# Kernel optimization log

Hardware: AMD Instinct MI355X
Metric: run time of the kernel (lower is better)

## Reference

```python
import jax, jax.numpy as jnp
import numpy as np

DIM = 1024
IMG_H, IMG_W = 512, 1408
CROP = 224
IMAGE_ORDER = (2, 0, 1, 5, 3, 4)
B, NC, NB = 2, 6, 32


def setup_inputs():
    key = jax.random.key(0)
    ks = jax.random.split(key, 12)
    camera_imgs = jax.random.normal(ks[0], (B, NC, 3, IMG_H, IMG_W), jnp.float32)
    u = jax.random.uniform(ks[1], (B, NB, 9), dtype=jnp.float32)
    centers = jnp.stack([u[..., 0] * 45.0 + 5.0,
                         (u[..., 1] - 0.5) * 40.0,
                         (u[..., 2] - 0.5) * 4.0], -1)
    pred_boxes = jnp.concatenate([centers, u[..., 3:] * 2.0], -1)  # [B,NB,9]
    K = np.array([[500., 0., IMG_W / 2.], [0., 500., IMG_H / 2.], [0., 0., 1.]])
    R_l2c = np.array([[0., -1., 0.], [0., 0., -1.], [1., 0., 0.]])  # lidar->camera axes
    mats = np.zeros((NC, 4, 4), np.float32)
    for c in range(NC):
        yaw = 2.0 * np.pi * c / NC
        Rz = np.array([[np.cos(yaw), -np.sin(yaw), 0.], [np.sin(yaw), np.cos(yaw), 0.], [0., 0., 1.]])
        mats[c, :3, :3] = K @ R_l2c @ Rz.T
        mats[c, 3, 3] = 1.0
    lidar2image = jnp.broadcast_to(jnp.asarray(mats), (B, NC, 4, 4))
    eye4 = jnp.eye(4, dtype=jnp.float32)
    img_aug_matrix = jnp.broadcast_to(eye4, (B, NC, 4, 4))
    lidar_aug_matrix = jnp.broadcast_to(eye4, (B, 4, 4))
    momentum = jnp.float32(0.5)
    box_default_dim = jax.random.normal(ks[2], (1, DIM), jnp.float32)
    theta_w = jnp.zeros((4, 9), jnp.float32)  # zero-init as in torch code
    theta_b = jnp.array([1., 0., 0., 1.], jnp.float32)

    def cw(k, shape):
        fan = shape[1] * shape[2] * shape[3]
        return jax.random.normal(k, shape, jnp.float32) * (2.0 / fan) ** 0.5
    conv1 = cw(ks[3], (64, 3, 7, 7))
    conv2 = cw(ks[4], (256, 64, 3, 3))
    conv3 = cw(ks[5], (DIM, 256, 3, 3))
    pos_embed = jax.random.normal(ks[6], (50, DIM), jnp.float32) * 0.02
    s = DIM ** -0.5
    wq = jax.random.normal(ks[7], (DIM, DIM), jnp.float32) * s
    wk = jax.random.normal(ks[8], (DIM, DIM), jnp.float32) * s
    wv = jax.random.normal(ks[9], (DIM, DIM), jnp.float32) * s
    wo = jax.random.normal(ks[10], (DIM, DIM), jnp.float32) * s
    return dict(camera_imgs=camera_imgs, pred_boxes=pred_boxes,
                img_aug_matrix=img_aug_matrix, lidar_aug_matrix=lidar_aug_matrix,
                lidar2image=lidar2image, momentum=momentum,
                box_default_dim=box_default_dim, theta_w=theta_w, theta_b=theta_b,
                conv1=conv1, conv2=conv2, conv3=conv3, pos_embed=pos_embed,
                wq=wq, wk=wk, wv=wv, wo=wo)


def _project(pred_boxes, lidar_aug_matrix, lidar2image, img_aug_matrix):
    # returns vu [B,NC,NB,2] = (row, col) pixel coords, on_img [B,NC,NB]
    def per_b(boxes, la, l2i, aug):
        c = boxes[:, :3] - la[:3, 3]                       # [NB,3]
        c = jnp.linalg.inv(la[:3, :3]) @ c.T               # [3,NB]
        c = l2i[:, :3, :3] @ c + l2i[:, :3, 3:4]           # [NC,3,NB]
        z = jnp.clip(c[:, 2], 1e-5, 1e5)
        xy = c[:, :2] / z[:, None]
        c = jnp.concatenate([xy, z[:, None]], 1)
        c = aug[:, :3, :3] @ c + aug[:, :3, 3:4]
        uv = c[:, :2].transpose(0, 2, 1)                   # [NC,NB,2] (col,row)
        vu = uv[..., ::-1]                                 # (row,col)
        on = (vu[..., 0] < IMG_H) & (vu[..., 0] >= 0) & (vu[..., 1] < IMG_W) & (vu[..., 1] >= 0)
        return vu, on
    return jax.vmap(per_b)(pred_boxes, lidar_aug_matrix, lidar2image, img_aug_matrix)


def _base_grid(h, w):
    # torch affine_grid align_corners=False pixel-center coords
    xs = (2.0 * jnp.arange(w) + 1.0) / w - 1.0
    ys = (2.0 * jnp.arange(h) + 1.0) / h - 1.0
    gx, gy = jnp.meshgrid(xs, ys)  # [h,w]
    return jnp.stack([gx, gy, jnp.ones_like(gx)], -1)  # [h,w,3]


def _grid_sample(img, grid):
    # img [C,H,W]; grid [...,2] xy in [-1,1]; bilinear, zeros padding, align_corners=False
    C, H, W = img.shape
    ix = ((grid[..., 0] + 1.0) * W - 1.0) / 2.0
    iy = ((grid[..., 1] + 1.0) * H - 1.0) / 2.0
    x0 = jnp.floor(ix); y0 = jnp.floor(iy)
    x1 = x0 + 1.0; y1 = y0 + 1.0
    wx = ix - x0; wy = iy - y0

    def gather(xx, yy):
        xi = jnp.clip(xx, 0, W - 1).astype(jnp.int32)
        yi = jnp.clip(yy, 0, H - 1).astype(jnp.int32)
        valid = (xx >= 0) & (xx <= W - 1) & (yy >= 0) & (yy <= H - 1)
        return img[:, yi, xi] * valid.astype(img.dtype)  # [C, ...]
    v00 = gather(x0, y0); v01 = gather(x1, y0)
    v10 = gather(x0, y1); v11 = gather(x1, y1)
    return (v00 * (1 - wx) * (1 - wy) + v01 * wx * (1 - wy)
            + v10 * (1 - wx) * wy + v11 * wx * wy)  # [C, ...]


def _clip_head(x, conv1, conv2, conv3, pos_embed, wq, wk, wv, wo):
    dn = ('NCHW', 'OIHW', 'NCHW')
    h = jax.nn.relu(jax.lax.conv_general_dilated(x, conv1, (4, 4), 'SAME', dimension_numbers=dn))
    h = jax.nn.relu(jax.lax.conv_general_dilated(h, conv2, (4, 4), 'SAME', dimension_numbers=dn))
    h = jax.nn.relu(jax.lax.conv_general_dilated(h, conv3, (2, 2), 'SAME', dimension_numbers=dn))  # [M,D,7,7]
    tok = h.reshape(h.shape[0], DIM, 49).transpose(0, 2, 1)              # [M,49,D]
    tok = jnp.concatenate([tok.mean(1, keepdims=True), tok], 1) + pos_embed  # [M,50,D]
    q = tok[:, :1] @ wq
    k = tok @ wk
    v = tok @ wv
    attn = jax.nn.softmax((q @ k.transpose(0, 2, 1)) * (DIM ** -0.5), -1)
    return ((attn @ v) @ wo)[:, 0]  # [M,D]


def reference(camera_imgs, pred_boxes, img_aug_matrix, lidar_aug_matrix, lidar2image,
              momentum, box_default_dim, theta_w, theta_b,
              conv1, conv2, conv3, pos_embed, wq, wk, wv, wo):
    N = B * NB
    vu, on_img = _project(pred_boxes, lidar_aug_matrix, lidar2image, img_aug_matrix)  # [B,NC,NB,2],[B,NC,NB]
    boxes_flat = pred_boxes.reshape(N, 9)
    rot = jnp.tanh(boxes_flat @ theta_w.T + theta_b).reshape(N, 2, 2)   # theta_rot MLP
    ty = vu[..., 0] / IMG_H * 2.0 - 1.0                                 # [B,NC,NB]
    tx = vu[..., 1] / IMG_W * 2.0 - 1.0
    pos = jnp.stack([tx, ty], -1).transpose(0, 2, 1, 3).reshape(N, NC, 2)
    theta = jnp.concatenate([jnp.broadcast_to(rot[:, None], (N, NC, 2, 2)),
                             pos[..., None]], -1)                        # [N,NC,2,3]
    base = _base_grid(CROP, CROP)                                        # [224,224,3]
    grids = jnp.einsum('hwk,ncjk->nchwj', base, theta)                   # [N,NC,224,224,2]
    grids = grids.reshape(B, NB, NC, CROP, CROP, 2)
    crops = []
    for b in range(B):
        for c in range(NC):
            smp = _grid_sample(camera_imgs[b, c], grids[b, :, c])        # [3,NB,224,224]
            crops.append(smp.transpose(1, 0, 2, 3))
    crops = jnp.stack(crops).reshape(B, NC, NB, 3, CROP, CROP)
    crops = crops.transpose(0, 2, 1, 3, 4, 5).reshape(N * NC, 3, CROP, CROP)
    emb = _clip_head(crops, conv1, conv2, conv3, pos_embed, wq, wk, wv, wo).reshape(N, NC, DIM)
    valid = on_img.transpose(0, 2, 1).reshape(N, NC)
    e = jnp.broadcast_to(box_default_dim, (N, DIM))
    for c in IMAGE_ORDER:  # sequential EMA over cameras, skipping off-image ones
        m = valid[:, c:c + 1]
        e = jnp.where(m, momentum * e + (1.0 - momentum) * emb[:, c], e)
    return e  # [N, DIM]
```

## Files before the change

### kernel.cpp

```cpp
#include <hip/hip_runtime.h>
#include <hip/hip_bf16.h>

#define DIMN 1024
#define IMG_H 512
#define IMG_W 1408
#define CROPN 224
#define NCAM 6
#define NBOXB 32
#define NBOX 64
#define NIMG 384

typedef __hip_bfloat16 bf16;
typedef unsigned short u16;
typedef float f32x4 __attribute__((ext_vector_type(4)));
typedef short bf16x8 __attribute__((ext_vector_type(8)));
typedef u16 u16x4 __attribute__((ext_vector_type(4)));
typedef u16 u16x8 __attribute__((ext_vector_type(8)));

__device__ __forceinline__ float b2f(bf16 x) { return __bfloat162float(x); }
__device__ __forceinline__ u16 f2us(float x) {
  bf16 h = __float2bfloat16(x);
  return *(u16*)&h;
}
__device__ __forceinline__ bf16x8 as_b(u16x8 x) {
  union { u16x8 u; bf16x8 b; } c; c.u = x; return c.b;
}

__global__ void k_w1r(const float* __restrict__ in, u16* __restrict__ out) {
  int idx = blockIdx.x * 256 + threadIdx.x;
  if (idx >= 64 * 224) return;
  int oc = idx / 224, t = idx % 224;
  int r = t >> 5, u = t & 31, kw = u >> 2, ch = u & 3;
  u16 v = (kw < 7 && ch < 3) ? f2us(in[((oc * 3 + ch) * 7 + r) * 7 + kw]) : (u16)0;
  out[(((oc >> 4) * 28 + (t >> 3)) * 16 + (oc & 15)) * 8 + (t & 7)] = v;
}
__global__ void k_w2r(const float* __restrict__ in, u16* __restrict__ out) {
  int idx = blockIdx.x * 256 + threadIdx.x;
  if (idx >= 256 * 576) return;
  int oc = idx / 576, t = idx % 576;
  int rk = t >> 6, ic = t & 63, r = rk / 3, kw = rk % 3;
  out[idx] = f2us(in[((oc * 64 + ic) * 3 + r) * 3 + kw]);
}
__global__ void k_w3r(const float* __restrict__ in, u16* __restrict__ out) {
  int idx = blockIdx.x * 256 + threadIdx.x;
  if (idx >= 1024 * 2304) return;
  int oc = idx / 2304, t = idx % 2304;
  int rk = t >> 8, ic = t & 255, r = rk / 3, kw = rk % 3;
  u16 v = f2us(in[((oc * 256 + ic) * 3 + r) * 3 + kw]);
  int ocb = oc >> 4, mm = oc & 15, kb = t >> 3, kj = t & 7;
  out[(((size_t)ocb * 288 + kb) * 16 + mm) * 8 + kj] = v;
}
__global__ void k_transpose_t(const float* __restrict__ w, float* __restrict__ wt) {
  __shared__ float tile[32][33];
  int x = blockIdx.x * 32 + threadIdx.x;
  for (int j = threadIdx.y; j < 32; j += 8)
    tile[j][threadIdx.x] = w[(size_t)(blockIdx.y * 32 + j) * 1024 + x];
  __syncthreads();
  int x2 = blockIdx.y * 32 + threadIdx.x;
  for (int j = threadIdx.y; j < 32; j += 8)
    wt[(size_t)(blockIdx.x * 32 + j) * 1024 + x2] = tile[threadIdx.x][j];
}

__global__ void k_proj(const float* __restrict__ boxes, const float* __restrict__ la_m,
                       const float* __restrict__ l2i, const float* __restrict__ aug,
                       const float* __restrict__ tw, const float* __restrict__ tb,
                       float* __restrict__ theta_out, int* __restrict__ valid_out) {
  int t = threadIdx.x;
  if (t >= NIMG) return;
  int n = t / NCAM, cam = t % NCAM;
  int b = n / NBOXB, nb = n % NBOXB;

  float la[4][4];
  for (int r = 0; r < 4; r++)
    for (int c = 0; c < 4; c++) la[r][c] = la_m[b * 16 + r * 4 + c];
  float a00=la[0][0],a01=la[0][1],a02=la[0][2];
  float a10=la[1][0],a11=la[1][1],a12=la[1][2];
  float a20=la[2][0],a21=la[2][1],a22=la[2][2];
  float c00 =  a11*a22 - a12*a21;
  float c01 = -(a10*a22 - a12*a20);
  float c02 =  a10*a21 - a11*a20;
  float det = a00*c00 + a01*c01 + a02*c02;
  float id = 1.0f / det;
  float inv[3][3];
  inv[0][0] = c00*id;                 inv[0][1] = -(a01*a22-a02*a21)*id;  inv[0][2] =  (a01*a12-a02*a11)*id;
  inv[1][0] = c01*id;                 inv[1][1] =  (a00*a22-a02*a20)*id;  inv[1][2] = -(a00*a12-a02*a10)*id;
  inv[2][0] = c02*id;                 inv[2][1] = -(a00*a21-a01*a20)*id;  inv[2][2] =  (a00*a11-a01*a10)*id;

  float bx[9];
  for (int i = 0; i < 9; i++) bx[i] = boxes[(b * NBOXB + nb) * 9 + i];
  float c0[3] = { bx[0]-la[0][3], bx[1]-la[1][3], bx[2]-la[2][3] };
  float c1[3];
  for (int r = 0; r < 3; r++) c1[r] = inv[r][0]*c0[0] + inv[r][1]*c0[1] + inv[r][2]*c0[2];

  const float* M = l2i + (size_t)(b * NCAM + cam) * 16;
  float p[3];
  for (int r = 0; r < 3; r++)
    p[r] = M[r*4+0]*c1[0] + M[r*4+1]*c1[1] + M[r*4+2]*c1[2] + M[r*4+3];
  float z = fminf(fmaxf(p[2], 1e-5f), 100000.0f);
  float x = p[0] / z, y = p[1] / z;
  const float* A = aug + (size_t)(b * NCAM + cam) * 16;
  float u = A[0]*x + A[1]*y + A[2]*z + A[3];
  float v = A[4]*x + A[5]*y + A[6]*z + A[7];

  int on = (v < (float)IMG_H) && (v >= 0.0f) && (u < (float)IMG_W) && (u >= 0.0f);
  float ty = v / (float)IMG_H * 2.0f - 1.0f;
  float tx = u / (float)IMG_W * 2.0f - 1.0f;

  float s[4];
  for (int j = 0; j < 4; j++) {
    float acc = tb[j];
    for (int i = 0; i < 9; i++) acc += tw[j * 9 + i] * bx[i];
    s[j] = tanhf(acc);
  }
  float* o = theta_out + t * 6;
  o[0] = s[0]; o[1] = s[1]; o[2] = tx;
  o[3] = s[2]; o[4] = s[3]; o[5] = ty;
  valid_out[t] = on;
}

#define HALO_PX 1356
__global__ void k_zero_halo(u16x4* __restrict__ c) {
  int t = blockIdx.x * 256 + threadIdx.x;
  int i = t / HALO_PX;
  if (i >= NIMG) return;
  int r = t % HALO_PX;
  int ph, pw;
  if (r < 684) {
    int rr = r / 228;
    ph = (rr == 0) ? 0 : (rr == 1 ? 225 : 226);
    pw = r % 228;
  } else {
    int q = r - 684;
    ph = 1 + q / 3;
    int s = q % 3;
    pw = (s == 0) ? 0 : (s == 1 ? 225 : 226);
  }
  c[(size_t)i * 228 * 228 + ph * 228 + pw] = (u16x4){0, 0, 0, 0};
}

__global__ __launch_bounds__(256) void k_sample(const float* __restrict__ imgs,
                                                const float* __restrict__ theta,
                                                u16* __restrict__ crops) {
  int idx = blockIdx.x * 256 + threadIdx.x;
  int i = idx / (CROPN * CROPN);
  int rem = idx - i * (CROPN * CROPN);
  int yy = rem / CROPN, xx = rem % CROPN;
  const float* th = theta + i * 6;
  float gx = (2.0f * xx + 1.0f) / (float)CROPN - 1.0f;
  float gy = (2.0f * yy + 1.0f) / (float)CROPN - 1.0f;
  float grid_x = th[0]*gx + th[1]*gy + th[2];
  float grid_y = th[3]*gx + th[4]*gy + th[5];
  float ix = ((grid_x + 1.0f) * (float)IMG_W - 1.0f) * 0.5f;
  float iy = ((grid_y + 1.0f) * (float)IMG_H - 1.0f) * 0.5f;
  float x0 = floorf(ix), y0 = floorf(iy);
  float wx = ix - x0, wy = iy - y0;
  int cam = i % NCAM, b = i / (NBOXB * NCAM);
  const float* base = imgs + (size_t)(b * NCAM + cam) * 3 * IMG_H * IMG_W;

  float xf[2] = { x0, x0 + 1.0f };
  float yf[2] = { y0, y0 + 1.0f };
  float wxa[2] = { 1.0f - wx, wx };
  float wya[2] = { 1.0f - wy, wy };
  int   xi[2], yi[2], vx[2], vy[2];
  for (int j = 0; j < 2; j++) {
    vx[j] = (xf[j] >= 0.0f) && (xf[j] <= (float)(IMG_W - 1));
    vy[j] = (yf[j] >= 0.0f) && (yf[j] <= (float)(IMG_H - 1));
    xi[j] = (int)fminf(fmaxf(xf[j], 0.0f), (float)(IMG_W - 1));
    yi[j] = (int)fminf(fmaxf(yf[j], 0.0f), (float)(IMG_H - 1));
  }
  float res[3];
  #pragma unroll
  for (int ch = 0; ch < 3; ch++) {
    const float* cp = base + (size_t)ch * IMG_H * IMG_W;
    float r = 0.0f;
    #pragma unroll
    for (int jy = 0; jy < 2; jy++)
      #pragma unroll
      for (int jx = 0; jx < 2; jx++) {
        float val = (vx[jx] && vy[jy]) ? cp[yi[jy] * IMG_W + xi[jx]] : 0.0f;
        r += val * wxa[jx] * wya[jy];
      }
    res[ch] = r;
  }
  u16x4 st = { f2us(res[0]), f2us(res[1]), f2us(res[2]), 0 };
  *(u16x4*)(crops + ((size_t)i * 228 * 228 + (size_t)(yy + 1) * 228 + (xx + 1)) * 4) = st;
}


#define C1_GROUPS 34
__global__ __launch_bounds__(256) void k_conv1m(const u16* __restrict__ X,
                                                const u16* __restrict__ W,
                                                u16* __restrict__ out) {
  __shared__ u16x8 sX[C1_GROUPS * 64];
  int blk = blockIdx.x;
  int i = blk / 14, rg = blk % 14;
  int tid = threadIdx.x, wv = tid >> 6, lane = tid & 63;
  int m = lane & 15, quad = lane >> 4;

  const u16* src = X + ((size_t)i * 51984 + (size_t)(rg * 16) * 228) * 4;
  #pragma unroll
  for (int j = 0; j < 9; j++) {
    int g = wv + j * 4;
    if (g < C1_GROUPS) {
      int c = g * 64 + lane;
      int cc = c < 2166 ? c : 2165;
      __builtin_amdgcn_global_load_lds(
          (const __attribute__((address_space(1))) void*)(src + (size_t)cc * 8),
          (__attribute__((address_space(3))) void*)(sX + g * 64),
          16, 0, 0);
    }
  }
  __syncthreads();

  int col[4];
  #pragma unroll
  for (int nt = 0; nt < 4; nt++) col[nt] = nt * 16 + m;
  f32x4 acc[4][4];
  #pragma unroll
  for (int t = 0; t < 4; t++)
    #pragma unroll
    for (int nt = 0; nt < 4; nt++) acc[t][nt] = (f32x4){0.f, 0.f, 0.f, 0.f};

  #pragma unroll
  for (int r = 0; r < 7; r++) {
    bf16x8 a[4];
    #pragma unroll
    for (int t = 0; t < 4; t++)
      a[t] = as_b(*(const u16x8*)(W + (size_t)(((t * 28 + r * 4 + quad) * 16 + m) * 8)));
    int lrow = wv * 4 + r;
    #pragma unroll
    for (int nt = 0; nt < 4; nt++) {
      int cl = col[nt] < 56 ? col[nt] : 55;
      bf16x8 bfr = as_b(sX[lrow * 114 + cl * 2 + quad]);
      #pragma unroll
      for (int t = 0; t < 4; t++)
        acc[t][nt] = __builtin_amdgcn_mfma_f32_16x16x32_bf16(a[t], bfr, acc[t][nt], 0, 0, 0);
    }
  }
  int oh = rg * 4 + wv;
  #pragma unroll
  for (int nt = 0; nt < 4; nt++) {
    if (col[nt] < 56) {
      int n = oh * 56 + col[nt];
      #pragma unroll
      for (int t = 0; t < 4; t++) {
        u16x4 st;
        #pragma unroll
        for (int r4 = 0; r4 < 4; r4++) st[r4] = f2us(fmaxf(acc[t][nt][r4], 0.f));
        *(u16x4*)(out + ((size_t)i * 3136 + n) * 64 + t * 16 + quad * 4) = st;
      }
    }
  }
}

__global__ __launch_bounds__(256) void k_conv2m(const u16* __restrict__ X,
                                                const u16* __restrict__ W,
                                                u16* __restrict__ out) {
  int blk = blockIdx.x;
  int i = blk >> 2, og = blk & 3;
  int oc0 = og * 64;
  int tid = threadIdx.x, wv = tid >> 6, lane = tid & 63;
  int m = lane & 15, quad = lane >> 4;
  int narr[4];
  const u16* bp[4];
  #pragma unroll
  for (int nt = 0; nt < 4; nt++) {
    int n = wv * 64 + nt * 16 + m;
    narr[nt] = n;
    int nc = n < 196 ? n : 195;
    int oh = nc / 14, ow = nc - oh * 14;
    bp[nt] = X + ((size_t)i * 3136 + (size_t)(oh * 4) * 56 + ow * 4) * 64 + quad * 8;
  }
  f32x4 acc[4][4];
  #pragma unroll
  for (int t = 0; t < 4; t++)
    #pragma unroll
    for (int nt = 0; nt < 4; nt++) acc[t][nt] = (f32x4){0.f, 0.f, 0.f, 0.f};

  #pragma unroll
  for (int s = 0; s < 18; s++) {
    const int rk = s >> 1, r = rk / 3, kw = rk % 3;
    const int boff = ((r * 56 + kw) * 64 + (s & 1) * 32);
    bf16x8 a[4];
    #pragma unroll
    for (int t = 0; t < 4; t++)
      a[t] = as_b(*(const u16x8*)(W + (size_t)(oc0 + t * 16 + m) * 576 + s * 32 + quad * 8));
    #pragma unroll
    for (int nt = 0; nt < 4; nt++) {
      bf16x8 bfr = as_b(*(const u16x8*)(bp[nt] + boff));
      #pragma unroll
      for (int t = 0; t < 4; t++)
        acc[t][nt] = __builtin_amdgcn_mfma_f32_16x16x32_bf16(a[t], bfr, acc[t][nt], 0, 0, 0);
    }
  }
  #pragma unroll
  for (int nt = 0; nt < 4; nt++) {
    int n = narr[nt];
    if (n < 196) {
      #pragma unroll
      for (int t = 0; t < 4; t++) {
        u16x4 st;
        #pragma unroll
        for (int r4 = 0; r4 < 4; r4++) st[r4] = f2us(fmaxf(acc[t][nt][r4], 0.f));
        *(u16x4*)(out + ((size_t)i * 196 + n) * 256 + oc0 + t * 16 + quad * 4) = st;
      }
    }
  }
}

__global__ __launch_bounds__(512, 2) void k_conv3m(const u16* __restrict__ X,
                                                   const u16* __restrict__ W,
                                                   float* __restrict__ out3) {
  __shared__ u16x8 sX8[6688];
  int bid = blockIdx.x;
  int og = (bid >> 2) & 1;
  int i  = (bid >> 3) * 4 + (bid & 3);
  int tid = threadIdx.x;

  const u16* src = X + (size_t)i * (196 * 256);
  u16x8 tmp[13];
  #pragma unroll
  for (int j = 0; j < 13; j++) {
    int c = tid + j * 512;
    int cc = c < 6272 ? c : 6271;
    tmp[j] = *(const u16x8*)(src + (size_t)cc * 8);
  }
  #pragma unroll
  for (int j = 0; j < 13; j++) {
    int c = tid + j * 512;
    int p = c >> 5, kc = c & 31;
    int ih = p / 14, iw = p - ih * 14;
    int gsw = ((iw >> 1) - (ih >> 1)) & 7;
    sX8[(c & ~31) | (kc ^ gsw)] = tmp[j];
  }
  if (tid < 32) sX8[6656 + tid] = (u16x8){0,0,0,0,0,0,0,0};
  __syncthreads();

  int wv = tid >> 6, lane = tid & 63;
  int m = lane & 15, quad = lane >> 4;
  int ocw = og * 512 + wv * 64;
  int narr[4], oh2[4], ow2[4];
  #pragma unroll
  for (int nt = 0; nt < 4; nt++) {
    int n = nt * 16 + m;
    narr[nt] = n;
    int nc = n < 49 ? n : 48;
    int oh = nc / 7, ow = nc - oh * 7;
    oh2[nt] = oh * 2; ow2[nt] = ow * 2;
  }
  f32x4 acc[4][4];
  #pragma unroll
  for (int t = 0; t < 4; t++)
    #pragma unroll
    for (int nt = 0; nt < 4; nt++) acc[t][nt] = (f32x4){0.f, 0.f, 0.f, 0.f};

  const u16* wbase = W + (size_t)(ocw >> 4) * (288 * 128) + m * 8;

  int bc[4], bk[4];
  auto set_bparams = [&](int rk) {
    const int r = rk / 3, kw = rk % 3;
    #pragma unroll
    for (int nt = 0; nt < 4; nt++) {
      int ih = oh2[nt] + r, iw = ow2[nt] + kw;
      bool valid = (narr[nt] < 49) && (ih < 14) && (iw < 14);
      int p = ih * 14 + iw;
      bc[nt] = valid ? p * 32 : 6656;
      bk[nt] = valid ? (((iw >> 1) - (ih >> 1)) & 7) : 0;
    }
  };
  auto loadA = [&](int t, int s) {
    return as_b(*(const u16x8*)(wbase + (size_t)(t * 288 + 4 * s + quad) * 128));
  };
  auto loadB = [&](int nt, int q4) {
    return as_b(sX8[bc[nt] + ((q4 + quad) ^ bk[nt])]);
  };

  bf16x8 A_[3][4], B_[2][4];
  set_bparams(0);
  #pragma unroll
  for (int t = 0; t < 4; t++) {
    A_[0][t] = loadA(t, 0);
    A_[1][t] = loadA(t, 1);
  }
  #pragma unroll
  for (int nt = 0; nt < 4; nt++) B_[0][nt] = loadB(nt, 0);

  #pragma unroll
  for (int s = 0; s < 72; s++) {
    if (s + 2 < 72) {
      #pragma unroll
      for (int t = 0; t < 4; t++) A_[(s + 2) % 3][t] = loadA(t, s + 2);
    }
    if (s + 1 < 72) {
      if (((s + 1) & 7) == 0) set_bparams((s + 1) >> 3);
      #pragma unroll
      for (int nt = 0; nt < 4; nt++) B_[(s + 1) & 1][nt] = loadB(nt, ((s + 1) & 7) * 4);
    }
    #pragma unroll
    for (int nt = 0; nt < 4; nt++)
      #pragma unroll
      for (int t = 0; t < 4; t++)
        acc[t][nt] = __builtin_amdgcn_mfma_f32_16x16x32_bf16(A_[s % 3][t], B_[s & 1][nt], acc[t][nt], 0, 0, 0);
  }

  #pragma unroll
  for (int nt = 0; nt < 4; nt++) {
    int n = narr[nt];
    if (n < 49) {
      #pragma unroll
      for (int t = 0; t < 4; t++) {
        f32x4 o;
        #pragma unroll
        for (int r4 = 0; r4 < 4; r4++) o[r4] = fmaxf(acc[t][nt][r4], 0.f);
        *(f32x4*)(out3 + ((size_t)i * 49 + n) * DIMN + ocw + t * 16 + quad * 4) = o;
      }
    }
  }
}

__global__ __launch_bounds__(256) void k_tok(const float* __restrict__ h,
                                             const float* __restrict__ pos,
                                             float* __restrict__ tok) {
  int blk = blockIdx.x;
  int i = blk / 50, t = blk % 50;
  int d = threadIdx.x * 4;
  float4 val;
  if (t == 0) {
    float sx = 0, sy = 0, sz = 0, sw = 0;
    for (int p = 0; p < 49; p++) {
      float4 v = *(const float4*)(h + ((size_t)i * 49 + p) * DIMN + d);
      sx += v.x; sy += v.y; sz += v.z; sw += v.w;
    }
    const float inv49 = 1.0f / 49.0f;
    val.x = sx * inv49; val.y = sy * inv49; val.z = sz * inv49; val.w = sw * inv49;
  } else {
    val = *(const float4*)(h + ((size_t)i * 49 + (t - 1)) * DIMN + d);
  }
  float4 pe = *(const float4*)(pos + (size_t)t * DIMN + d);
  float4 o; o.x = val.x + pe.x; o.y = val.y + pe.y; o.z = val.z + pe.z; o.w = val.w + pe.w;
  *(float4*)(tok + ((size_t)i * 50 + t) * DIMN + d) = o;
}

__global__ __launch_bounds__(256) void k_matvec2(const float* __restrict__ vecs, int vstride,
                                                 const float* __restrict__ M,
                                                 float* __restrict__ out) {
  __shared__ float s_v[4][DIMN];
  int i0 = blockIdx.x * 4;
  int h = blockIdx.y;
  for (int e = threadIdx.x; e < 4 * DIMN; e += 256)
    s_v[e >> 10][e & 1023] = vecs[(size_t)(i0 + (e >> 10)) * vstride + (e & 1023)];
  __syncthreads();
  int d0 = h * 512 + threadIdx.x * 2;
  float2 acc[4] = {{0,0},{0,0},{0,0},{0,0}};
  for (int e = 0; e < DIMN; e++) {
    float2 w = *(const float2*)(M + (size_t)e * DIMN + d0);
    #pragma unroll
    for (int im = 0; im < 4; im++) {
      float x = s_v[im][e];
      acc[im].x += x * w.x; acc[im].y += x * w.y;
    }
  }
  #pragma unroll
  for (int im = 0; im < 4; im++)
    *(float2*)(out + (size_t)(i0 + im) * DIMN + d0) = acc[im];
}

__global__ __launch_bounds__(256) void k_attn(const float* __restrict__ tok,
                                              const float* __restrict__ a1,
                                              float* __restrict__ tvec) {
  __shared__ float s_a[DIMN];
  __shared__ float s_sc[50];
  __shared__ float s_at[50];
  int i = blockIdx.x;
  for (int e = threadIdx.x; e < DIMN; e += 256) s_a[e] = a1[(size_t)i * DIMN + e];
  __syncthreads();
  int wave = threadIdx.x >> 6, lane = threadIdx.x & 63;
  for (int t = wave; t < 50; t += 4) {
    const float* tr = tok + ((size_t)i * 50 + t) * DIMN;
    float p = 0.0f;
    for (int mm = 0; mm < 16; mm++) {
      int e = lane + mm * 64;
      p += tr[e] * s_a[e];
    }
    for (int off = 32; off > 0; off >>= 1) p += __shfl_down(p, off, 64);
    if (lane == 0) s_sc[t] = p * 0.03125f;
  }
  __syncthreads();
  if (threadIdx.x == 0) {
    float mx = s_sc[0];
    for (int t = 1; t < 50; t++) mx = fmaxf(mx, s_sc[t]);
    float sum = 0.0f;
    for (int t = 0; t < 50; t++) { float ex = expf(s_sc[t] - mx); s_at[t] = ex; sum += ex; }
    float inv = 1.0f / sum;
    for (int t = 0; t < 50; t++) s_at[t] *= inv;
  }
  __syncthreads();
  int d0 = threadIdx.x * 4;
  float ax = 0, ay = 0, az = 0, aw = 0;
  for (int t = 0; t < 50; t++) {
    float at = s_at[t];
    float4 tv = *(const float4*)(tok + ((size_t)i * 50 + t) * DIMN + d0);
    ax += at * tv.x; ay += at * tv.y; az += at * tv.z; aw += at * tv.w;
  }
  float4 o; o.x = ax; o.y = ay; o.z = az; o.w = aw;
  *(float4*)(tvec + (size_t)i * DIMN + d0) = o;
}

__global__ void k_final(const float* __restrict__ emb,
                        const int* __restrict__ valid,
                        const float* __restrict__ bdd,
                        const float* __restrict__ momp,
                        float* __restrict__ out) {
  int n = blockIdx.x;
  int d0 = threadIdx.x * 4;
  float mom = momp[0];
  float e[4];
  #pragma unroll
  for (int j = 0; j < 4; j++) e[j] = bdd[d0 + j];
  const int order[6] = {2, 0, 1, 5, 3, 4};
  #pragma unroll
  for (int s = 0; s < 6; s++) {
    int c = order[s];
    int i = n * NCAM + c;
    if (valid[i]) {
      const float* er = emb + (size_t)i * DIMN + d0;
      #pragma unroll
      for (int j = 0; j < 4; j++) e[j] = mom * e[j] + (1.0f - mom) * er[j];
    }
  }
  #pragma unroll
  for (int j = 0; j < 4; j++) out[(size_t)n * DIMN + d0 + j] = e[j];
}

extern "C" void kernel_launch(void* const* d_in, const int* in_sizes, int n_in,
                              void* d_out, int out_size, void* d_ws, size_t ws_size,
                              hipStream_t stream) {
  const float* in_cam = (const float*)d_in[0];
  const float* in_box = (const float*)d_in[1];
  const float* in_aug = (const float*)d_in[2];
  const float* in_la  = (const float*)d_in[3];
  const float* in_l2i = (const float*)d_in[4];
  const float* in_mom = (const float*)d_in[5];
  const float* in_bdd = (const float*)d_in[6];
  const float* in_tw  = (const float*)d_in[7];
  const float* in_tb  = (const float*)d_in[8];
  const float* in_c1  = (const float*)d_in[9];
  const float* in_c2  = (const float*)d_in[10];
  const float* in_c3  = (const float*)d_in[11];
  const float* in_pe  = (const float*)d_in[12];
  const float* in_wq  = (const float*)d_in[13];
  const float* in_wk  = (const float*)d_in[14];
  const float* in_wv  = (const float*)d_in[15];
  const float* in_wo  = (const float*)d_in[16];

  char* base = (char*)d_ws;
  size_t off = 0;
  auto carve = [&](size_t bytes) -> char* {
    char* p = base + off;
    off += (bytes + 255) & ~(size_t)255;
    return p;
  };
  float* theta   = (float*)carve((size_t)NIMG * 6 * 4);
  int*   valid   = (int*)carve((size_t)NIMG * 4);
  float* qbuf    = (float*)carve((size_t)NIMG * DIMN * 4);
  float* a1buf   = (float*)carve((size_t)NIMG * DIMN * 4);
  float* tvbuf   = (float*)carve((size_t)NIMG * DIMN * 4);
  float* ctxbuf  = (float*)carve((size_t)NIMG * DIMN * 4);
  float* embbuf  = (float*)carve((size_t)NIMG * DIMN * 4);
  float* wkT_f   = (float*)carve((size_t)DIMN * DIMN * 4);
  u16*   W1r     = (u16*)carve((size_t)64 * 224 * 2);
  u16*   W2r     = (u16*)carve((size_t)256 * 576 * 2);
  u16*   W3r     = (u16*)carve((size_t)1024 * 2304 * 2);
  u16*   c2o     = (u16*)carve((size_t)NIMG * 196 * 256 * 2);
  char*  R1      = carve((size_t)NIMG * 228 * 228 * 4 * 2);
  u16*   c1o     = (u16*)carve((size_t)NIMG * 3136 * 64 * 2);
  u16*   crops   = (u16*)R1;
  float* conv3o  = (float*)R1;
  float* tok     = (float*)(R1 + (size_t)NIMG * 49 * DIMN * 4);

  k_w1r<<<56, 256, 0, stream>>>(in_c1, W1r);
  k_w2r<<<576, 256, 0, stream>>>(in_c2, W2r);
  k_w3r<<<9216, 256, 0, stream>>>(in_c3, W3r);
  k_transpose_t<<<dim3(32, 32), dim3(32, 8), 0, stream>>>(in_wk, wkT_f);

  k_proj<<<1, 384, 0, stream>>>(in_box, in_la, in_l2i, in_aug, in_tw, in_tb, theta, valid);
  k_zero_halo<<<(NIMG * HALO_PX + 255) / 256, 256, 0, stream>>>((u16x4*)crops);
  k_sample<<<(NIMG * CROPN * CROPN) / 256, 256, 0, stream>>>(in_cam, theta, crops);
  k_conv1m<<<NIMG * 14, 256, 0, stream>>>(crops, W1r, c1o);
  k_conv2m<<<NIMG * 4, 256, 0, stream>>>(c1o, W2r, c2o);
  k_conv3m<<<768, 512, 0, stream>>>(c2o, W3r, conv3o);
  k_tok<<<NIMG * 50, 256, 0, stream>>>(conv3o, in_pe, tok);
  k_matvec2<<<dim3(96, 2), 256, 0, stream>>>(tok, 50 * DIMN, in_wq, qbuf);
  k_matvec2<<<dim3(96, 2), 256, 0, stream>>>(qbuf, DIMN, wkT_f, a1buf);
  k_attn<<<NIMG, 256, 0, stream>>>(tok, a1buf, tvbuf);
  k_matvec2<<<dim3(96, 2), 256, 0, stream>>>(tvbuf, DIMN, in_wv, ctxbuf);
  k_matvec2<<<dim3(96, 2), 256, 0, stream>>>(ctxbuf, DIMN, in_wo, embbuf);
  k_final<<<NBOX, 256, 0, stream>>>(embbuf, valid, in_bdd, in_mom, (float*)d_out);
}
```

Measured before the change: 986.0 us.

## Stage conv2 input in swizzled LDS with MFMA-friendly weight layout

conv2 is restructured so each block covers one image and a band of output rows for all 256 channels. It loads the relevant input rows into LDS with an XOR swizzle and reads weights from a new blocked layout in place of the old strided global gathers. Triple-buffered A/B register prefetch is added. conv3 gets a 16-way swizzle and precomputed per-tap offsets so B-parameter math no longer runs in the main loop. The cost is more registers for the offset tables, which may reduce occupancy.

```diff
diff --git a/kernel.cpp b/kernel.cpp
--- a/kernel.cpp
+++ b/kernel.cpp
@@ -39,7 +39,8 @@
   if (idx >= 256 * 576) return;
   int oc = idx / 576, t = idx % 576;
   int rk = t >> 6, ic = t & 63, r = rk / 3, kw = rk % 3;
-  out[idx] = f2us(in[((oc * 64 + ic) * 3 + r) * 3 + kw]);
+  u16 v = f2us(in[((oc * 64 + ic) * 3 + r) * 3 + kw]);
+  out[(((oc >> 4) * 72 + (t >> 3)) * 16 + (oc & 15)) * 8 + (t & 7)] = v;
 }
 __global__ void k_w3r(const float* __restrict__ in, u16* __restrict__ out) {
   int idx = blockIdx.x * 256 + threadIdx.x;
@@ -253,56 +254,98 @@
   }
 }
 
-__global__ __launch_bounds__(256) void k_conv2m(const u16* __restrict__ X,
-                                                const u16* __restrict__ W,
-                                                u16* __restrict__ out) {
-  int blk = blockIdx.x;
-  int i = blk >> 2, og = blk & 3;
-  int oc0 = og * 64;
+__global__ __launch_bounds__(256, 3) void k_conv2m(const u16* __restrict__ X,
+                                                   const u16* __restrict__ W,
+                                                   u16* __restrict__ out) {
+  __shared__ u16x8 s2[3136];
+  int bid = blockIdx.x;
+  int i = bid / 7, ohg = bid % 7;
   int tid = threadIdx.x, wv = tid >> 6, lane = tid & 63;
   int m = lane & 15, quad = lane >> 4;
-  int narr[4];
-  const u16* bp[4];
-  #pragma unroll
-  for (int nt = 0; nt < 4; nt++) {
-    int n = wv * 64 + nt * 16 + m;
-    narr[nt] = n;
-    int nc = n < 196 ? n : 195;
-    int oh = nc / 14, ow = nc - oh * 14;
-    bp[nt] = X + ((size_t)i * 3136 + (size_t)(oh * 4) * 56 + ow * 4) * 64 + quad * 8;
-  }
-  f32x4 acc[4][4];
+
+  const u16* src = X + ((size_t)i * 3136 + 8 * ohg * 56) * 64;
+  u16x8 tmp[13];
+  #pragma unroll
+  for (int j = 0; j < 13; j++) {
+    int c = tid + j * 256;
+    int cc = c < 3136 ? c : 3135;
+    tmp[j] = *(const u16x8*)(src + (size_t)cc * 8);
+  }
+  #pragma unroll
+  for (int j = 0; j < 13; j++) {
+    int c = tid + j * 256;
+    int cc = c < 3136 ? c : 3135;
+    int pixel = cc >> 3;
+    int li = pixel / 56, iw = pixel - li * 56;
+    int g = (14 * (li >> 2) + (iw >> 2)) & 15;
+    s2[(cc & ~15) | ((cc ^ g) & 15)] = tmp[j];
+  }
+  __syncthreads();
+
+  int nl[2], pk2[9][2];
+  #pragma unroll
+  for (int nt = 0; nt < 2; nt++) {
+    int n = nt * 16 + m;
+    nl[nt] = n;
+    int nc = n < 28 ? n : 27;
+    int ohl = nc / 14, ow = nc - ohl * 14;
+    int g = nc & 15;
+    #pragma unroll
+    for (int rk = 0; rk < 9; rk++) {
+      int r = rk / 3, kw = rk % 3;
+      int pixel = (ohl * 4 + r) * 56 + (ow * 4 + kw);
+      int cb = pixel * 8;
+      int base2 = (cb & ~15) | ((cb & 8) ^ (g & 8));
+      pk2[rk][nt] = base2 | (g & 7);
+    }
+  }
+  f32x4 acc[4][2];
   #pragma unroll
   for (int t = 0; t < 4; t++)
     #pragma unroll
-    for (int nt = 0; nt < 4; nt++) acc[t][nt] = (f32x4){0.f, 0.f, 0.f, 0.f};
+    for (int nt = 0; nt < 2; nt++) acc[t][nt] = (f32x4){0.f, 0.f, 0.f, 0.f};
+
+  const u16* wbase = W + (size_t)(wv * 4) * (72 * 128) + m * 8;
+  auto loadA = [&](int t, int s) {
+    return as_b(*(const u16x8*)(wbase + (size_t)(t * 72 + s * 4 + quad) * 128));
+  };
+  auto loadB = [&](int nt, int s) {
+    int pkv = pk2[s >> 1][nt];
+    int sub = (s & 1) * 4 + quad;
+    return as_b(s2[(pkv & ~7) | (sub ^ (pkv & 7))]);
+  };
+
+  bf16x8 A_[3][4], B_[3][2];
+  #pragma unroll
+  for (int t = 0; t < 4; t++) { A_[0][t] = loadA(t, 0); A_[1][t] = loadA(t, 1); }
+  #pragma unroll
+  for (int nt = 0; nt < 2; nt++) { B_[0][nt] = loadB(nt, 0); B_[1][nt] = loadB(nt, 1); }
 
   #pragma unroll
   for (int s = 0; s < 18; s++) {
-    const int rk = s >> 1, r = rk / 3, kw = rk % 3;
-    const int boff = ((r * 56 + kw) * 64 + (s & 1) * 32);
-    bf16x8 a[4];
-    #pragma unroll
-    for (int t = 0; t < 4; t++)
-      a[t] = as_b(*(const u16x8*)(W + (size_t)(oc0 + t * 16 + m) * 576 + s * 32 + quad * 8));
-    #pragma unroll
-    for (int nt = 0; nt < 4; nt++) {
-      bf16x8 bfr = as_b(*(const u16x8*)(bp[nt] + boff));
+    if (s + 2 < 18) {
+      #pragma unroll
+      for (int t = 0; t < 4; t++) A_[(s + 2) % 3][t] = loadA(t, s + 2);
+      #pragma unroll
+      for (int nt = 0; nt < 2; nt++) B_[(s + 2) % 3][nt] = loadB(nt, s + 2);
+    }
+    #pragma unroll
+    for (int nt = 0; nt < 2; nt++)
       #pragma unroll
       for (int t = 0; t < 4; t++)
-        acc[t][nt] = __builtin_amdgcn_mfma_f32_16x16x32_bf16(a[t], bfr, acc[t][nt], 0, 0, 0);
-    }
-  }
-  #pragma unroll
-  for (int nt = 0; nt < 4; nt++) {
-    int n = narr[nt];
-    if (n < 196) {
+        acc[t][nt] = __builtin_amdgcn_mfma_f32_16x16x32_bf16(A_[s % 3][t], B_[s % 3][nt], acc[t][nt], 0, 0, 0);
+  }
+
+  #pragma unroll
+  for (int nt = 0; nt < 2; nt++) {
+    if (nl[nt] < 28) {
+      int n = ohg * 28 + nl[nt];
       #pragma unroll
       for (int t = 0; t < 4; t++) {
         u16x4 st;
         #pragma unroll
         for (int r4 = 0; r4 < 4; r4++) st[r4] = f2us(fmaxf(acc[t][nt][r4], 0.f));
-        *(u16x4*)(out + ((size_t)i * 196 + n) * 256 + oc0 + t * 16 + quad * 4) = st;
+        *(u16x4*)(out + ((size_t)i * 196 + n) * 256 + wv * 64 + t * 16 + quad * 4) = st;
       }
     }
   }
@@ -328,10 +371,10 @@
   #pragma unroll
   for (int j = 0; j < 13; j++) {
     int c = tid + j * 512;
-    int p = c >> 5, kc = c & 31;
+    int p = c >> 5;
     int ih = p / 14, iw = p - ih * 14;
-    int gsw = ((iw >> 1) - (ih >> 1)) & 7;
-    sX8[(c & ~31) | (kc ^ gsw)] = tmp[j];
+    int g = (7 * (ih >> 1) + (iw >> 1)) & 15;
+    sX8[(c & ~15) | ((c ^ g) & 15)] = tmp[j];
   }
   if (tid < 32) sX8[6656 + tid] = (u16x8){0,0,0,0,0,0,0,0};
   __syncthreads();
@@ -348,59 +391,55 @@
     int oh = nc / 7, ow = nc - oh * 7;
     oh2[nt] = oh * 2; ow2[nt] = ow * 2;
   }
-  f32x4 acc[4][4];
-  #pragma unroll
-  for (int t = 0; t < 4; t++)
-    #pragma unroll
-    for (int nt = 0; nt < 4; nt++) acc[t][nt] = (f32x4){0.f, 0.f, 0.f, 0.f};
-
-  const u16* wbase = W + (size_t)(ocw >> 4) * (288 * 128) + m * 8;
-
-  int bc[4], bk[4];
-  auto set_bparams = [&](int rk) {
-    const int r = rk / 3, kw = rk % 3;
+  int pk[9][4];
+  #pragma unroll
+  for (int rk = 0; rk < 9; rk++) {
+    int r = rk / 3, kw = rk % 3;
     #pragma unroll
     for (int nt = 0; nt < 4; nt++) {
       int ih = oh2[nt] + r, iw = ow2[nt] + kw;
       bool valid = (narr[nt] < 49) && (ih < 14) && (iw < 14);
       int p = ih * 14 + iw;
-      bc[nt] = valid ? p * 32 : 6656;
-      bk[nt] = valid ? (((iw >> 1) - (ih >> 1)) & 7) : 0;
-    }
-  };
+      int g = (7 * (ih >> 1) + (iw >> 1)) & 15;
+      pk[rk][nt] = valid ? (((p * 32) << 4) | g) : (6656 << 4);
+    }
+  }
+  f32x4 acc[4][4];
+  #pragma unroll
+  for (int t = 0; t < 4; t++)
+    #pragma unroll
+    for (int nt = 0; nt < 4; nt++) acc[t][nt] = (f32x4){0.f, 0.f, 0.f, 0.f};
+
+  const u16* wbase = W + (size_t)(ocw >> 4) * (288 * 128) + m * 8;
+
   auto loadA = [&](int t, int s) {
     return as_b(*(const u16x8*)(wbase + (size_t)(t * 288 + 4 * s + quad) * 128));
   };
-  auto loadB = [&](int nt, int q4) {
-    return as_b(sX8[bc[nt] + ((q4 + quad) ^ bk[nt])]);
+  auto loadB = [&](int nt, int s) {
+    int pkv = pk[s >> 3][nt];
+    int q = (s & 7) * 4 + quad;
+    return as_b(sX8[(pkv >> 4) + (q ^ (pkv & 15))]);
   };
 
-  bf16x8 A_[3][4], B_[2][4];
-  set_bparams(0);
-  #pragma unroll
-  for (int t = 0; t < 4; t++) {
-    A_[0][t] = loadA(t, 0);
-    A_[1][t] = loadA(t, 1);
-  }
-  #pragma unroll
-  for (int nt = 0; nt < 4; nt++) B_[0][nt] = loadB(nt, 0);
+  bf16x8 A_[3][4], B_[3][4];
+  #pragma unroll
+  for (int t = 0; t < 4; t++) { A_[0][t] = loadA(t, 0); A_[1][t] = loadA(t, 1); }
+  #pragma unroll
+  for (int nt = 0; nt < 4; nt++) { B_[0][nt] = loadB(nt, 0); B_[1][nt] = loadB(nt, 1); }
 
   #pragma unroll
   for (int s = 0; s < 72; s++) {
     if (s + 2 < 72) {
       #pragma unroll
       for (int t = 0; t < 4; t++) A_[(s + 2) % 3][t] = loadA(t, s + 2);
-    }
-    if (s + 1 < 72) {
-      if (((s + 1) & 7) == 0) set_bparams((s + 1) >> 3);
-      #pragma unroll
-      for (int nt = 0; nt < 4; nt++) B_[(s + 1) & 1][nt] = loadB(nt, ((s + 1) & 7) * 4);
+      #pragma unroll
+      for (int nt = 0; nt < 4; nt++) B_[(s + 2) % 3][nt] = loadB(nt, s + 2);
     }
     #pragma unroll
     for (int nt = 0; nt < 4; nt++)
       #pragma unroll
       for (int t = 0; t < 4; t++)
-        acc[t][nt] = __builtin_amdgcn_mfma_f32_16x16x32_bf16(A_[s % 3][t], B_[s & 1][nt], acc[t][nt], 0, 0, 0);
+        acc[t][nt] = __builtin_amdgcn_mfma_f32_16x16x32_bf16(A_[s % 3][t], B_[s % 3][nt], acc[t][nt], 0, 0, 0);
   }
 
   #pragma unroll
@@ -587,7 +626,7 @@
   k_zero_halo<<<(NIMG * HALO_PX + 255) / 256, 256, 0, stream>>>((u16x4*)crops);
   k_sample<<<(NIMG * CROPN * CROPN) / 256, 256, 0, stream>>>(in_cam, theta, crops);
   k_conv1m<<<NIMG * 14, 256, 0, stream>>>(crops, W1r, c1o);
-  k_conv2m<<<NIMG * 4, 256, 0, stream>>>(c1o, W2r, c2o);
+  k_conv2m<<<NIMG * 7, 256, 0, stream>>>(c1o, W2r, c2o);
   k_conv3m<<<768, 512, 0, stream>>>(c2o, W3r, conv3o);
   k_tok<<<NIMG * 50, 256, 0, stream>>>(conv3o, in_pe, tok);
   k_matvec2<<<dim3(96, 2), 256, 0, stream>>>(tok, 50 * DIMN, in_wq, qbuf);
```

Measured after the change: 951.7 us. 3.5% less time.
